# Kernel optimization log

Hardware: AMD Instinct MI355X
Metric: run time of the kernel (lower is better)

The kernel has to match this reference:

```python
import jax, jax.numpy as jnp
import numpy as np

H = 16           # num_heads
D = 1024         # num_units
QD = KD = VD = 64
LN_EPS = 1e-5


def _xavier(key, shape):
    fan_in, fan_out = shape[-2], shape[-1]
    std = np.sqrt(2.0 / (fan_in + fan_out))
    return jax.random.normal(key, shape, dtype=jnp.float32) * std


def setup_inputs() -> dict:
    key = jax.random.key(0)
    ks = jax.random.split(key, 10)
    B, Sq, Sk = 8, 1024, 1024
    return {
        "query": jax.random.normal(ks[0], (B, Sq, D), dtype=jnp.float32),
        "keys": jax.random.normal(ks[1], (B, Sk, D), dtype=jnp.float32),
        "values": jax.random.normal(ks[2], (B, Sk, D), dtype=jnp.float32),
        "Wq": _xavier(ks[3], (H, D, QD)),
        "Wk": _xavier(ks[4], (H, D, KD)),
        "Wv": _xavier(ks[5], (H, D, VD)),
        "Wp": _xavier(ks[6], (H * VD, D)),   # proj, stored input-major: y = x @ Wp + bp
        "bp": jnp.zeros((D,), dtype=jnp.float32),
        "gamma": jnp.ones((D,), dtype=jnp.float32),
        "beta": jnp.zeros((D,), dtype=jnp.float32),
    }


def reference(query, keys, values, Wq, Wk, Wv, Wp, bp, gamma, beta):
    B, Sq, _ = query.shape
    Sk = keys.shape[1]
    # RepeatLinear per head: [B,S,D] x [H,D,e] -> [H,B,S,e]
    Q = jnp.einsum("bsd,hde->hbse", query, Wq)
    K = jnp.einsum("bsd,hde->hbse", keys, Wk)
    V = jnp.einsum("bsd,hde->hbse", values, Wv)
    # NOTE: original scales by sqrt(num_units), not sqrt(key_dim)
    temper = jnp.asarray(np.sqrt(D), dtype=Q.dtype)
    scores = jnp.einsum("hbqe,hbke->hbqk", Q, K) / temper  # [H,B,Sq,Sk]
    attn = jax.nn.softmax(scores, axis=-1)
    # dropout is identity in eval mode
    out = jnp.einsum("hbqk,hbke->hbqe", attn, V)           # [H,B,Sq,VD]
    # torch.cat(torch.split(out, B, 0), -1): head-major feature concat
    out = out.transpose(1, 2, 0, 3).reshape(B, Sq, H * VD)
    out = out @ Wp + bp                                     # proj
    # residual + LayerNorm
    y = out + query
    mu = jnp.mean(y, axis=-1, keepdims=True)
    var = jnp.var(y, axis=-1, keepdims=True)
    y = (y - mu) / jnp.sqrt(var + LN_EPS) * gamma + beta
    return y, attn.reshape(H * B, Sq, Sk)
```

## Files before the change

kernel.cpp:

```cpp
#include <hip/hip_runtime.h>
#include <hip/hip_bf16.h>

#define H_ 16
#define B_ 8
#define S_ 1024
#define D_ 1024
#define E_ 64
#define HB_ 128
#define LN_EPS 1e-5f
#define LOG2E 1.4426950408889634f

typedef unsigned short u16;
typedef __bf16 bf16x8 __attribute__((ext_vector_type(8)));
typedef u16 u16x8 __attribute__((ext_vector_type(8)));
typedef u16 u16x4 __attribute__((ext_vector_type(4)));
typedef float f32x4 __attribute__((ext_vector_type(4)));
typedef unsigned u32x2 __attribute__((ext_vector_type(2)));

#define MFMA16(a, b, c) __builtin_amdgcn_mfma_f32_16x16x32_bf16( \
    __builtin_bit_cast(bf16x8, (a)), __builtin_bit_cast(bf16x8, (b)), (c), 0, 0, 0)

#define GLL16(gp, lp) __builtin_amdgcn_global_load_lds( \
    (const __attribute__((address_space(1))) void*)(gp), \
    (__attribute__((address_space(3))) void*)(lp), 16, 0, 0)

__device__ __forceinline__ unsigned cvt_pk_bf16(float lo, float hi) {
  unsigned r;
  asm("v_cvt_pk_bf16_f32 %0, %1, %2" : "=v"(r) : "v"(lo), "v"(hi));
  return r;
}
__device__ __forceinline__ u16x4 pk4(f32x4 v) {
  union { unsigned u[2]; u16x4 s; } r;
  r.u[0] = cvt_pk_bf16(v[0], v[1]);
  r.u[1] = cvt_pk_bf16(v[2], v[3]);
  return r.s;
}
__device__ __forceinline__ float exp2_hw(float x) {
  float r;
  asm("v_exp_f32 %0, %1" : "=v"(r) : "v"(x));
  return r;
}
__device__ __forceinline__ float bfhi(unsigned u) {
  return __builtin_bit_cast(float, u & 0xFFFF0000u);
}
__device__ __forceinline__ float bflo(unsigned u) {
  return __builtin_bit_cast(float, u << 16);
}

__global__ __launch_bounds__(256) void k_prep(
    const float* __restrict__ Wq, const float* __restrict__ Wk,
    const float* __restrict__ Wv, const float* __restrict__ Wp,
    u16* __restrict__ Wt,
    const float* __restrict__ Xq, const float* __restrict__ Xk,
    const float* __restrict__ Xv, u16* __restrict__ Xdst) {
  const int bid = blockIdx.x;
  if (bid >= 1024) {
    const int b2 = bid - 1024;
    const int t = b2 >> 12;
    const float* X = t == 0 ? Xq : t == 1 ? Xk : Xv;
    u16* Y = Xdst + (size_t)t * (8 << 20);
    int i = ((b2 & 4095) * 256 + threadIdx.x) * 8;
    f32x4 a = *(const f32x4*)(X + i);
    f32x4 b = *(const f32x4*)(X + i + 4);
    union { unsigned u[4]; u16x8 s; } v;
    v.u[0] = cvt_pk_bf16(a[0], a[1]);
    v.u[1] = cvt_pk_bf16(a[2], a[3]);
    v.u[2] = cvt_pk_bf16(b[0], b[1]);
    v.u[3] = cvt_pk_bf16(b[2], b[3]);
    *(u16x8*)(Y + i) = v.s;
    return;
  }
  __shared__ float tile[64][65];
  const int which = bid >> 8, r = bid & 255;
  const float* src;
  int R, C, rt, ct;
  float scale = 1.0f;
  size_t soff, doff;
  if (which < 3) {
    src = which == 0 ? Wq : which == 1 ? Wk : Wv;
    if (which == 0) scale = LOG2E / 32.0f;
    int slice = r & 15, rtile = r >> 4;
    R = 1024; C = 64; rt = rtile * 64; ct = 0;
    soff = (size_t)slice * 65536;
    doff = (size_t)which * (1 << 20) + (size_t)slice * 65536;
  } else {
    src = Wp;
    R = 1024; C = 1024; rt = (r & 15) * 64; ct = (r >> 4) * 64;
    soff = 0; doff = (size_t)3 * (1 << 20);
  }
  const float* I = src + soff;
  u16* O = Wt + doff;
  const int t = threadIdx.x;
  const int c4 = (t & 15) * 4;
  #pragma unroll
  for (int i = 0; i < 4; i++) {
    int rr = i * 16 + (t >> 4);
    f32x4 v = *(const f32x4*)&I[(size_t)(rt + rr) * C + ct + c4];
    tile[rr][c4 + 0] = v[0]; tile[rr][c4 + 1] = v[1];
    tile[rr][c4 + 2] = v[2]; tile[rr][c4 + 3] = v[3];
  }
  __syncthreads();
  #pragma unroll
  for (int i = 0; i < 4; i++) {
    int oc = i * 16 + (t >> 4);
    f32x4 tv;
    #pragma unroll
    for (int rr = 0; rr < 4; rr++) tv[rr] = tile[c4 + rr][oc] * scale;
    *(u16x4*)&O[(size_t)(ct + oc) * R + rt + c4] = pk4(tv);
  }
}

#define STAGE_TILES() do { \
    GLL16(Ag + kt,             AsB0); \
    GLL16(Ag + 64 * 1024 + kt, AsB0 + 2048); \
    GLL16(Bg + kt,             BsB0); \
    GLL16(Bg + 64 * 1024 + kt, BsB0 + 2048); \
  } while (0)

#define READ_FRAGS() do { \
    _Pragma("unroll") \
    for (int mi = 0; mi < 4; mi++) \
      af[mi] = *(const u16x8*)&As[(wr * 64 + mi * 16 + lr) * 32 + lg * 8]; \
    _Pragma("unroll") \
    for (int ni = 0; ni < 4; ni++) \
      bf[ni] = *(const u16x8*)&Bs[(wc * 64 + ni * 16 + lr) * 32 + lg * 8]; \
  } while (0)

template<int MODE>
__global__ __launch_bounds__(256) void k_gemm(
    const u16* __restrict__ X0, const u16* __restrict__ Ball,
    u16* __restrict__ O0, u16* __restrict__ O1, u16* __restrict__ O2,
    float* __restrict__ Pf, const float* __restrict__ bp,
    const float* __restrict__ query) {
  const int bid = blockIdx.x + (blockIdx.y << 6);
  const int bx  = ((bid & 7) << 3) + ((bid >> 3) & 7);
  const int by  = bid >> 6;
  const int l  = threadIdx.x & 63;
  const int w  = threadIdx.x >> 6;
  const int lr = l & 15, lg = l >> 4;
  const int wr = w >> 1, wc = w & 1;
  const int m0 = bx * 128, n0 = by * 128;

  const u16* A = (MODE == 0) ? X0 + (size_t)(by >> 3) * (8 << 20) : X0;

  __shared__ __align__(16) u16 As[128 * 32];
  __shared__ __align__(16) u16 Bs[128 * 32];

  const int srow = w * 16 + (l >> 2);
  const int scol = (l & 3) * 8;
  const u16* Ag = A    + (size_t)(m0 + srow) * 1024 + scol;
  const u16* Bg = Ball + (size_t)(n0 + srow) * 1024 + scol;
  u16* AsB0 = As + w * 512;
  u16* BsB0 = Bs + w * 512;

  f32x4 acc[4][4] = {};
  u16x8 af[4], bf[4];

  if (MODE == 2 || by < 16) {
    for (int kt = 0; kt < 1024; kt += 32) {
      STAGE_TILES();
      __syncthreads();
      READ_FRAGS();
      #pragma unroll
      for (int mi = 0; mi < 4; mi++)
        #pragma unroll
        for (int ni = 0; ni < 4; ni++)
          acc[mi][ni] = MFMA16(bf[ni], af[mi], acc[mi][ni]);
      __syncthreads();
    }
  } else {
    for (int kt = 0; kt < 1024; kt += 32) {
      STAGE_TILES();
      __syncthreads();
      READ_FRAGS();
      #pragma unroll
      for (int mi = 0; mi < 4; mi++)
        #pragma unroll
        for (int ni = 0; ni < 4; ni++)
          acc[mi][ni] = MFMA16(af[mi], bf[ni], acc[mi][ni]);
      __syncthreads();
    }
  }

  if (MODE == 0 && by < 16) {
    u16* Out = (by >= 8) ? O1 : O0;
    const int h = (by & 7) * 2 + wc;
    #pragma unroll
    for (int mi = 0; mi < 4; mi++) {
      int s = m0 + wr * 64 + mi * 16 + lr;
      int bb = s >> 10, ss = s & 1023;
      #pragma unroll
      for (int ni = 0; ni < 4; ni++)
        *(u16x4*)&Out[((size_t)(h * 8 + bb) * 1024 + ss) * 64 + ni * 16 + lg * 4] =
            pk4(acc[mi][ni]);
    }
  } else if (MODE == 0) {
    const int byv = by - 16;
    const int h = byv * 2 + wc;
    #pragma unroll
    for (int mi = 0; mi < 4; mi++) {
      int s = m0 + wr * 64 + mi * 16 + lg * 4;
      int bb = s >> 10, ss = s & 1023;
      #pragma unroll
      for (int ni = 0; ni < 4; ni++)
        *(u16x4*)&O2[((size_t)(h * 8 + bb) * 64 + ni * 16 + lr) * 1024 + ss] =
            pk4(acc[mi][ni]);
    }
  } else {
    #pragma unroll
    for (int mi = 0; mi < 4; mi++) {
      int m = m0 + wr * 64 + mi * 16 + lr;
      #pragma unroll
      for (int ni = 0; ni < 4; ni++) {
        int n = n0 + wc * 64 + ni * 16 + lg * 4;
        f32x4 b4 = *(const f32x4*)(bp + n);
        f32x4 q4 = *(const f32x4*)(query + (size_t)m * 1024 + n);
        f32x4 o = acc[mi][ni] + b4 + q4;
        *(f32x4*)(Pf + (size_t)m * 1024 + n) = o;
      }
    }
  }
}

__global__ __launch_bounds__(256, 4) void k_attn(const u16* __restrict__ Qb,
    const u16* __restrict__ Kb, const u16* __restrict__ Vtb,
    float* __restrict__ attn_out, u16* __restrict__ AO) {
  const int bid = blockIdx.x;
  const int xcd = bid & 7, within = bid >> 3;
  const int qt = within & 63;
  const int hb = xcd * 16 + (within >> 6);
  const int w  = threadIdx.x >> 6;
  const int l  = threadIdx.x & 63;
  const int lr = l & 15, lg = l >> 4;
  const int q0 = qt * 16;

  __shared__ __align__(16) u16 pbuf[16 * 1024];
  __shared__ float wmaxs[4][16];
  __shared__ float wsums[4][16];

  const u16* Qp = Qb + ((size_t)hb * 1024 + q0 + lr) * 64 + lg * 8;
  const u16* Kp = Kb + ((size_t)hb * 1024 + w * 256 + lr) * 64 + lg * 8;
  u16x8 q_lo = *(const u16x8*)Qp;
  u16x8 q_hi = *(const u16x8*)(Qp + 32);

  f32x4 sacc[16] = {};
  __builtin_amdgcn_s_setprio(1);
  #pragma unroll
  for (int j = 0; j < 16; j++) {
    u16x8 k0 = *(const u16x8*)(Kp + (size_t)j * 16 * 64);
    u16x8 k1 = *(const u16x8*)(Kp + (size_t)j * 16 * 64 + 32);
    sacc[j] = MFMA16(k0, q_lo, sacc[j]);
    sacc[j] = MFMA16(k1, q_hi, sacc[j]);
  }
  __builtin_amdgcn_s_setprio(0);

  float mx = sacc[0][0];
  #pragma unroll
  for (int j = 0; j < 16; j++)
    #pragma unroll
    for (int r = 0; r < 4; r++) mx = fmaxf(mx, sacc[j][r]);
  mx = fmaxf(mx, __shfl_xor(mx, 16));
  mx = fmaxf(mx, __shfl_xor(mx, 32));

  float sum = 0.f;
  #pragma unroll
  for (int j = 0; j < 16; j++)
    #pragma unroll
    for (int r = 0; r < 4; r++) {
      float p = exp2_hw(sacc[j][r] - mx);
      sacc[j][r] = p;
      sum += p;
    }
  sum += __shfl_xor(sum, 16);
  sum += __shfl_xor(sum, 32);

  const u16* Vp = Vtb + ((size_t)hb * 64 + w * 16 + lr) * 1024 + lg * 8;
  u16x8 vp0 = *(const u16x8*)(Vp + 0);
  u16x8 vp1 = *(const u16x8*)(Vp + 32);
  u16x8 vp2 = *(const u16x8*)(Vp + 64);
  u16x8 vp3 = *(const u16x8*)(Vp + 96);

  #pragma unroll
  for (int j = 0; j < 16; j++) {
    int k0 = w * 256 + j * 16 + lg * 4;
    int byte = (lr * 2048 + k0 * 2) ^ ((lr & 7) << 4);
    *(u16x4*)((char*)pbuf + byte) = pk4(sacc[j]);
  }
  if (l < 16) { wmaxs[w][lr] = mx; wsums[w][lr] = sum; }

  __syncthreads();

  float m0v = wmaxs[0][lr], m1v = wmaxs[1][lr], m2v = wmaxs[2][lr], m3v = wmaxs[3][lr];
  float gmax = fmaxf(fmaxf(m0v, m1v), fmaxf(m2v, m3v));
  float e0 = exp2_hw(m0v - gmax), e1 = exp2_hw(m1v - gmax);
  float e2 = exp2_hw(m2v - gmax), e3 = exp2_hw(m3v - gmax);
  float gsum = wsums[0][lr] * e0 + wsums[1][lr] * e1 + wsums[2][lr] * e2 + wsums[3][lr] * e3;
  float inv = 1.0f / gsum;
  float c0 = e0 * inv, c1 = e1 * inv, c2 = e2 * inv, c3 = e3 * inv;
  float scale_own = exp2_hw(mx - gmax) * inv;

  f32x4 o0 = {}, o1 = {}, o2 = {}, o3 = {};
  __builtin_amdgcn_s_setprio(1);
  #pragma unroll
  for (int i = 0; i < 4; i++)
    #pragma unroll
    for (int kk = 0; kk < 8; kk++) {
      int kb = i * 256 + kk * 32 + lg * 8;
      int byte = (lr * 2048 + kb * 2) ^ ((lr & 7) << 4);
      u16x8 p = *(u16x8*)((char*)pbuf + byte);
      u16x8 v;
      if (i == 0 && kk == 0) v = vp0;
      else if (i == 0 && kk == 1) v = vp1;
      else if (i == 0 && kk == 2) v = vp2;
      else if (i == 0 && kk == 3) v = vp3;
      else v = *(const u16x8*)(Vp + i * 256 + kk * 32);
      if (i == 0) o0 = MFMA16(v, p, o0);
      else if (i == 1) o1 = MFMA16(v, p, o1);
      else if (i == 2) o2 = MFMA16(v, p, o2);
      else o3 = MFMA16(v, p, o3);
    }
  __builtin_amdgcn_s_setprio(0);

  const int bb = hb & 7, hh = hb >> 3;
  f32x4 oc;
  #pragma unroll
  for (int r = 0; r < 4; r++)
    oc[r] = o0[r] * c0 + o1[r] * c1 + o2[r] * c2 + o3[r] * c3;
  *(u16x4*)&AO[((size_t)bb * 1024 + q0 + lr) * 1024 + hh * 64 + w * 16 + lg * 4] = pk4(oc);

  float* Ap = attn_out + ((size_t)hb * 1024 + q0 + lr) * 1024 + w * 256 + lg * 4;
  #pragma unroll
  for (int j = 0; j < 16; j++) {
    int k0 = w * 256 + j * 16 + lg * 4;
    int byte = (lr * 2048 + k0 * 2) ^ ((lr & 7) << 4);
    u32x2 d = *(u32x2*)((char*)pbuf + byte);
    f32x4 v;
    v[0] = bflo(d[0]) * scale_own;
    v[1] = bfhi(d[0]) * scale_own;
    v[2] = bflo(d[1]) * scale_own;
    v[3] = bfhi(d[1]) * scale_own;
    __builtin_nontemporal_store(v, (f32x4*)(Ap + j * 16));
  }
}

__global__ __launch_bounds__(256) void k_ln(const float* __restrict__ P,
    const float* __restrict__ gamma, const float* __restrict__ beta,
    float* __restrict__ y) {
  const int row = blockIdx.x * 4 + (threadIdx.x >> 6);
  const int l = threadIdx.x & 63;
  const float* p = P + (size_t)row * 1024 + l * 4;
  f32x4 v[4];
  float s = 0.f, s2 = 0.f;
  #pragma unroll
  for (int i = 0; i < 4; i++) {
    v[i] = *(const f32x4*)(p + i * 256);
    #pragma unroll
    for (int r = 0; r < 4; r++) { s += v[i][r]; s2 += v[i][r] * v[i][r]; }
  }
  #pragma unroll
  for (int off = 1; off < 64; off <<= 1) {
    s += __shfl_xor(s, off);
    s2 += __shfl_xor(s2, off);
  }
  float mu = s * (1.0f / 1024.0f);
  float var = s2 * (1.0f / 1024.0f) - mu * mu;
  float rstd = rsqrtf(var + LN_EPS);
  float* yp = y + (size_t)row * 1024 + l * 4;
  #pragma unroll
  for (int i = 0; i < 4; i++) {
    f32x4 g = *(const f32x4*)(gamma + l * 4 + i * 256);
    f32x4 b = *(const f32x4*)(beta + l * 4 + i * 256);
    f32x4 o;
    #pragma unroll
    for (int r = 0; r < 4; r++) o[r] = (v[i][r] - mu) * rstd * g[r] + b[r];
    __builtin_nontemporal_store(o, (f32x4*)(yp + i * 256));
  }
}

extern "C" void kernel_launch(void* const* d_in, const int* in_sizes, int n_in,
                              void* d_out, int out_size, void* d_ws, size_t ws_size,
                              hipStream_t stream) {
  const float* query  = (const float*)d_in[0];
  const float* keys   = (const float*)d_in[1];
  const float* values = (const float*)d_in[2];
  const float* Wq     = (const float*)d_in[3];
  const float* Wk     = (const float*)d_in[4];
  const float* Wv     = (const float*)d_in[5];
  const float* Wp     = (const float*)d_in[6];
  const float* bp     = (const float*)d_in[7];
  const float* gamma  = (const float*)d_in[8];
  const float* beta   = (const float*)d_in[9];

  float* y        = (float*)d_out;
  float* attn_out = (float*)d_out + (size_t)B_ * S_ * D_;

  u16* ws  = (u16*)d_ws;
  u16* Wqt = ws;
  u16* Wpt = Wqt + (3 << 20);
  u16* Xqb = Wqt + (4 << 20);
  u16* Qb  = Xqb + (24 << 20);
  u16* Kb  = Qb + (8 << 20);
  u16* Vtb = Kb + (8 << 20);
  u16* AO  = Vtb + (8 << 20);
  float* P = (float*)Xqb;

  k_prep<<<13312, 256, 0, stream>>>(Wq, Wk, Wv, Wp, Wqt, query, keys, values, Xqb);

  k_gemm<0><<<dim3(64, 24), 256, 0, stream>>>(Xqb, Wqt, Qb, Kb, Vtb, nullptr, nullptr, nullptr);

  k_attn<<<8192, 256, 0, stream>>>(Qb, Kb, Vtb, attn_out, AO);

  k_gemm<2><<<dim3(64, 8), 256, 0, stream>>>(AO, Wpt, nullptr, nullptr, nullptr, P, bp, query);
  k_ln<<<2048, 256, 0, stream>>>(P, gamma, beta, y);
}
```

Before: 421.2 us.

## Split attention block across eight waves with two-way split-K PV reduction

```diff
diff --git a/kernel.cpp b/kernel.cpp
--- a/kernel.cpp
+++ b/kernel.cpp
@@ -15,6 +15,7 @@
 typedef u16 u16x8 __attribute__((ext_vector_type(8)));
 typedef u16 u16x4 __attribute__((ext_vector_type(4)));
 typedef float f32x4 __attribute__((ext_vector_type(4)));
+typedef float f32x2 __attribute__((ext_vector_type(2)));
 typedef unsigned u32x2 __attribute__((ext_vector_type(2)));
 
 #define MFMA16(a, b, c) __builtin_amdgcn_mfma_f32_16x16x32_bf16( \
@@ -222,7 +223,7 @@
   }
 }
 
-__global__ __launch_bounds__(256, 4) void k_attn(const u16* __restrict__ Qb,
+__global__ __launch_bounds__(512, 6) void k_attn(const u16* __restrict__ Qb,
     const u16* __restrict__ Kb, const u16* __restrict__ Vtb,
     float* __restrict__ attn_out, u16* __restrict__ AO) {
   const int bid = blockIdx.x;
@@ -235,18 +236,19 @@
   const int q0 = qt * 16;
 
   __shared__ __align__(16) u16 pbuf[16 * 1024];
-  __shared__ float wmaxs[4][16];
-  __shared__ float wsums[4][16];
+  __shared__ float wmaxs[8][16];
+  __shared__ float wsums[8][16];
+  __shared__ __align__(16) f32x4 xbuf[4][64];
 
   const u16* Qp = Qb + ((size_t)hb * 1024 + q0 + lr) * 64 + lg * 8;
-  const u16* Kp = Kb + ((size_t)hb * 1024 + w * 256 + lr) * 64 + lg * 8;
+  const u16* Kp = Kb + ((size_t)hb * 1024 + w * 128 + lr) * 64 + lg * 8;
   u16x8 q_lo = *(const u16x8*)Qp;
   u16x8 q_hi = *(const u16x8*)(Qp + 32);
 
-  f32x4 sacc[16] = {};
+  f32x4 sacc[8] = {};
   __builtin_amdgcn_s_setprio(1);
   #pragma unroll
-  for (int j = 0; j < 16; j++) {
+  for (int j = 0; j < 8; j++) {
     u16x8 k0 = *(const u16x8*)(Kp + (size_t)j * 16 * 64);
     u16x8 k1 = *(const u16x8*)(Kp + (size_t)j * 16 * 64 + 32);
     sacc[j] = MFMA16(k0, q_lo, sacc[j]);
@@ -256,7 +258,7 @@
 
   float mx = sacc[0][0];
   #pragma unroll
-  for (int j = 0; j < 16; j++)
+  for (int j = 0; j < 8; j++)
     #pragma unroll
     for (int r = 0; r < 4; r++) mx = fmaxf(mx, sacc[j][r]);
   mx = fmaxf(mx, __shfl_xor(mx, 16));
@@ -264,7 +266,7 @@
 
   float sum = 0.f;
   #pragma unroll
-  for (int j = 0; j < 16; j++)
+  for (int j = 0; j < 8; j++)
     #pragma unroll
     for (int r = 0; r < 4; r++) {
       float p = exp2_hw(sacc[j][r] - mx);
@@ -274,15 +276,9 @@
   sum += __shfl_xor(sum, 16);
   sum += __shfl_xor(sum, 32);
 
-  const u16* Vp = Vtb + ((size_t)hb * 64 + w * 16 + lr) * 1024 + lg * 8;
-  u16x8 vp0 = *(const u16x8*)(Vp + 0);
-  u16x8 vp1 = *(const u16x8*)(Vp + 32);
-  u16x8 vp2 = *(const u16x8*)(Vp + 64);
-  u16x8 vp3 = *(const u16x8*)(Vp + 96);
-
-  #pragma unroll
-  for (int j = 0; j < 16; j++) {
-    int k0 = w * 256 + j * 16 + lg * 4;
+  #pragma unroll
+  for (int j = 0; j < 8; j++) {
+    int k0 = w * 128 + j * 16 + lg * 4;
     int byte = (lr * 2048 + k0 * 2) ^ ((lr & 7) << 4);
     *(u16x4*)((char*)pbuf + byte) = pk4(sacc[j]);
   }
@@ -291,55 +287,72 @@
   __syncthreads();
 
   float m0v = wmaxs[0][lr], m1v = wmaxs[1][lr], m2v = wmaxs[2][lr], m3v = wmaxs[3][lr];
-  float gmax = fmaxf(fmaxf(m0v, m1v), fmaxf(m2v, m3v));
-  float e0 = exp2_hw(m0v - gmax), e1 = exp2_hw(m1v - gmax);
-  float e2 = exp2_hw(m2v - gmax), e3 = exp2_hw(m3v - gmax);
-  float gsum = wsums[0][lr] * e0 + wsums[1][lr] * e1 + wsums[2][lr] * e2 + wsums[3][lr] * e3;
+  float m4v = wmaxs[4][lr], m5v = wmaxs[5][lr], m6v = wmaxs[6][lr], m7v = wmaxs[7][lr];
+  float gmax = fmaxf(fmaxf(fmaxf(m0v, m1v), fmaxf(m2v, m3v)),
+                     fmaxf(fmaxf(m4v, m5v), fmaxf(m6v, m7v)));
+  float gsum = wsums[0][lr] * exp2_hw(m0v - gmax) + wsums[1][lr] * exp2_hw(m1v - gmax)
+             + wsums[2][lr] * exp2_hw(m2v - gmax) + wsums[3][lr] * exp2_hw(m3v - gmax)
+             + wsums[4][lr] * exp2_hw(m4v - gmax) + wsums[5][lr] * exp2_hw(m5v - gmax)
+             + wsums[6][lr] * exp2_hw(m6v - gmax) + wsums[7][lr] * exp2_hw(m7v - gmax);
   float inv = 1.0f / gsum;
-  float c0 = e0 * inv, c1 = e1 * inv, c2 = e2 * inv, c3 = e3 * inv;
-  float scale_own = exp2_hw(mx - gmax) * inv;
-
-  f32x4 o0 = {}, o1 = {}, o2 = {}, o3 = {};
+
+  const int t = w & 3, half = w >> 2;
+  const int sb = half * 4;
+  float ms0 = wmaxs[sb + 0][lr], ms1 = wmaxs[sb + 1][lr];
+  float ms2 = wmaxs[sb + 2][lr], ms3 = wmaxs[sb + 3][lr];
+  const u16* Vp = Vtb + ((size_t)hb * 64 + t * 16 + lr) * 1024 + lg * 8;
+
+  f32x4 o = {};
   __builtin_amdgcn_s_setprio(1);
-  #pragma unroll
-  for (int i = 0; i < 4; i++)
-    #pragma unroll
-    for (int kk = 0; kk < 8; kk++) {
-      int kb = i * 256 + kk * 32 + lg * 8;
-      int byte = (lr * 2048 + kb * 2) ^ ((lr & 7) << 4);
-      u16x8 p = *(u16x8*)((char*)pbuf + byte);
-      u16x8 v;
-      if (i == 0 && kk == 0) v = vp0;
-      else if (i == 0 && kk == 1) v = vp1;
-      else if (i == 0 && kk == 2) v = vp2;
-      else if (i == 0 && kk == 3) v = vp3;
-      else v = *(const u16x8*)(Vp + i * 256 + kk * 32);
-      if (i == 0) o0 = MFMA16(v, p, o0);
-      else if (i == 1) o1 = MFMA16(v, p, o1);
-      else if (i == 2) o2 = MFMA16(v, p, o2);
-      else o3 = MFMA16(v, p, o3);
-    }
+  #define PBUF_P(s, kk) (*(u16x8*)((char*)pbuf + \
+      ((lr * 2048 + ((s) * 128 + (kk) * 32 + lg * 8) * 2) ^ ((lr & 7) << 4))))
+  #pragma unroll
+  for (int kk = 0; kk < 4; kk++) o = MFMA16(*(const u16x8*)(Vp + (sb+0)*128 + kk*32), PBUF_P(sb+0, kk), o);
+  o *= exp2_hw(ms0 - ms1);
+  #pragma unroll
+  for (int kk = 0; kk < 4; kk++) o = MFMA16(*(const u16x8*)(Vp + (sb+1)*128 + kk*32), PBUF_P(sb+1, kk), o);
+  o *= exp2_hw(ms1 - ms2);
+  #pragma unroll
+  for (int kk = 0; kk < 4; kk++) o = MFMA16(*(const u16x8*)(Vp + (sb+2)*128 + kk*32), PBUF_P(sb+2, kk), o);
+  o *= exp2_hw(ms2 - ms3);
+  #pragma unroll
+  for (int kk = 0; kk < 4; kk++) o = MFMA16(*(const u16x8*)(Vp + (sb+3)*128 + kk*32), PBUF_P(sb+3, kk), o);
   __builtin_amdgcn_s_setprio(0);
+  #undef PBUF_P
+  o *= exp2_hw(ms3 - gmax) * inv;
+
+  if (half == 1) xbuf[t][l] = o;
+  __syncthreads();
 
   const int bb = hb & 7, hh = hb >> 3;
-  f32x4 oc;
-  #pragma unroll
-  for (int r = 0; r < 4; r++)
-    oc[r] = o0[r] * c0 + o1[r] * c1 + o2[r] * c2 + o3[r] * c3;
-  *(u16x4*)&AO[((size_t)bb * 1024 + q0 + lr) * 1024 + hh * 64 + w * 16 + lg * 4] = pk4(oc);
-
-  float* Ap = attn_out + ((size_t)hb * 1024 + q0 + lr) * 1024 + w * 256 + lg * 4;
-  #pragma unroll
-  for (int j = 0; j < 16; j++) {
-    int k0 = w * 256 + j * 16 + lg * 4;
-    int byte = (lr * 2048 + k0 * 2) ^ ((lr & 7) << 4);
-    u32x2 d = *(u32x2*)((char*)pbuf + byte);
-    f32x4 v;
-    v[0] = bflo(d[0]) * scale_own;
-    v[1] = bfhi(d[0]) * scale_own;
-    v[2] = bflo(d[1]) * scale_own;
-    v[3] = bfhi(d[1]) * scale_own;
-    __builtin_nontemporal_store(v, (f32x4*)(Ap + j * 16));
+  if (half == 0) {
+    f32x4 oc = o + xbuf[t][l];
+    *(u16x4*)&AO[((size_t)bb * 1024 + q0 + lr) * 1024 + hh * 64 + t * 16 + lg * 4] = pk4(oc);
+  }
+
+  #pragma unroll
+  for (int rr = 0; rr < 2; rr++) {
+    const int row = w * 2 + rr;
+    float M[8];
+    #pragma unroll
+    for (int i = 0; i < 8; i++) M[i] = wmaxs[i][row];
+    float GM = fmaxf(fmaxf(fmaxf(M[0], M[1]), fmaxf(M[2], M[3])),
+                     fmaxf(fmaxf(M[4], M[5]), fmaxf(M[6], M[7])));
+    float GS = 0.f;
+    #pragma unroll
+    for (int i = 0; i < 8; i++) GS += wsums[i][row] * exp2_hw(M[i] - GM);
+    float IV = 1.0f / GS;
+    float* Ap = attn_out + ((size_t)hb * 1024 + q0 + row) * 1024;
+    #pragma unroll
+    for (int c = 0; c < 8; c++) {
+      float sc = exp2_hw(M[c] - GM) * IV;
+      int byte = (row * 2048 + c * 256 + l * 4) ^ ((row & 7) << 4);
+      unsigned d = *(unsigned*)((char*)pbuf + byte);
+      f32x2 v;
+      v[0] = bflo(d) * sc;
+      v[1] = bfhi(d) * sc;
+      __builtin_nontemporal_store(v, (f32x2*)(Ap + c * 128 + l * 2));
+    }
   }
 }
 
@@ -408,7 +421,7 @@
 
   k_gemm<0><<<dim3(64, 24), 256, 0, stream>>>(Xqb, Wqt, Qb, Kb, Vtb, nullptr, nullptr, nullptr);
 
-  k_attn<<<8192, 256, 0, stream>>>(Qb, Kb, Vtb, attn_out, AO);
+  k_attn<<<8192, 512, 0, stream>>>(Qb, Kb, Vtb, attn_out, AO);
 
   k_gemm<2><<<dim3(64, 8), 256, 0, stream>>>(AO, Wpt, nullptr, nullptr, nullptr, P, bp, query);
   k_ln<<<2048, 256, 0, stream>>>(P, gamma, beta, y);
```

Result: faster. 400.7 us (-4.9%).
